# Kernel tuning notes

Hardware: AMD Instinct MI355X
Metric: run time of the kernel (lower is better)

Reference implementation:

```python
import jax, jax.numpy as jnp
import numpy as np

COMMITMENT_COST = 0.25
NUM_EMBEDDINGS = 512
EMBEDDING_DIM = 128


def setup_inputs() -> dict:
    key = jax.random.key(0)
    k1, k2 = jax.random.split(key)
    z = jax.random.normal(k1, (64, 128, 32, 32), dtype=jnp.float32)
    # nn.Embedding weight initialized uniform(-1/K, 1/K)
    lim = 1.0 / NUM_EMBEDDINGS
    emb_weight = jax.random.uniform(
        k2, (NUM_EMBEDDINGS, EMBEDDING_DIM), dtype=jnp.float32,
        minval=-lim, maxval=lim)
    return {"z": z, "emb_weight": emb_weight}


def reference(z, emb_weight):
    b, c, h, w = z.shape  # c == embedding_dim
    # (b, h, w, c) -> (b*h*w, c)
    z_cl = jnp.transpose(z, (0, 2, 3, 1))
    z_flat = z_cl.reshape(b * h * w, c)
    # squared L2 distances: ||z||^2 + ||e||^2 - 2 z.e  -> [N, K]
    distances = (
        jnp.sum(z_flat ** 2, axis=-1, keepdims=True)
        + jnp.sum(emb_weight ** 2, axis=-1)[None, :]
        - 2.0 * jnp.matmul(z_flat, emb_weight.T)
    )
    encoding_indices = jnp.argmin(distances, axis=-1)  # [N]
    z_q = emb_weight[encoding_indices]                 # [N, c]
    z_q = z_q.reshape(b, h, w, c)
    z_q = jnp.transpose(z_q, (0, 3, 1, 2))             # [b, c, h, w]
    loss = (
        jnp.mean((z_q - jax.lax.stop_gradient(z)) ** 2)
        + COMMITMENT_COST * jnp.mean((jax.lax.stop_gradient(z_q) - z) ** 2)
    )
    # straight-through estimator
    z_q_st = z + jax.lax.stop_gradient(z_q - z)
    return (z_q_st, loss, encoding_indices)
```

## Files before the change

### kernel.cpp

```cpp
#include <hip/hip_runtime.h>


#define D_DIM 128
#define HW    1024
#define GAP_THR 2.5e-4f
#define FLAG_CAP 16384

typedef short short8 __attribute__((ext_vector_type(8)));
typedef float f32x16 __attribute__((ext_vector_type(16)));

union U8 { unsigned int u[4]; short8 s; uint4 q; };

__device__ __forceinline__ unsigned short f2bf(float v) {
    unsigned int u = __builtin_bit_cast(unsigned int, v);
    return (unsigned short)((u + 0x7fffu + ((u >> 16) & 1u)) >> 16);
}
__device__ __forceinline__ float bfhi(unsigned short h) {
    unsigned int u = ((unsigned int)h) << 16;
    return __builtin_bit_cast(float, u);
}
__device__ __forceinline__ unsigned int umn(unsigned int a, unsigned int b) {
    return a < b ? a : b;
}
__device__ __forceinline__ unsigned int umx(unsigned int a, unsigned int b) {
    return a > b ? a : b;
}

__global__ void prep_kernel(const float* __restrict__ emb,
                            float* __restrict__ etr,
                            uint4* __restrict__ ebh, uint4* __restrict__ ebl,
                            float* __restrict__ se) {
    const int t = blockIdx.x * 256 + threadIdx.x;

    {
        const int k = t >> 7;
        const int d = t & 127;
        etr[d * 512 + k] = emb[t];
    }

    if (t < 8192) {
        const int lane = t & 63;
        const int ks   = (t >> 6) & 7;
        const int kcol = t >> 9;
        const int krow = kcol * 32 + (lane & 31);
        const int d0   = ks * 16 + (lane >> 5) * 8;
        const float* ep = emb + (size_t)krow * D_DIM + d0;
        float v[8];
        #pragma unroll
        for (int j = 0; j < 8; ++j) v[j] = ep[j];
        U8 hh, ll;
        #pragma unroll
        for (int p = 0; p < 4; ++p) {
            const unsigned short h0 = f2bf(v[2*p]), h1 = f2bf(v[2*p+1]);
            const unsigned short l0 = f2bf(v[2*p]   - bfhi(h0));
            const unsigned short l1 = f2bf(v[2*p+1] - bfhi(h1));
            hh.u[p] = (unsigned int)h0 | ((unsigned int)h1 << 16);
            ll.u[p] = (unsigned int)l0 | ((unsigned int)l1 << 16);
        }
        ebh[t] = hh.q;
        ebl[t] = ll.q;
    }

    if (t < 512) {
        const float* e = emb + (size_t)t * D_DIM;
        float r[8];
        #pragma unroll
        for (int j = 0; j < 8; ++j) {
            float v = e[j];
            float p = v * v;
            asm("" : "+v"(p));
            r[j] = p;
        }
        for (int i = 8; i < 128; i += 8) {
            #pragma unroll
            for (int j = 0; j < 8; ++j) {
                float v = e[i + j];
                float p = v * v;
                asm("" : "+v"(p));
                r[j] += p;
            }
        }
        se[t] = ((r[0] + r[1]) + (r[2] + r[3])) + ((r[4] + r[5]) + (r[6] + r[7]));
    }
}

__launch_bounds__(256, 1)
__global__ void dist_kernel(const float* __restrict__ z,
                            const uint4* __restrict__ ebh,
                            const uint4* __restrict__ ebl,
                            const float* __restrict__ se_g,
                            const float* __restrict__ emb,
                            float* __restrict__ idx_out,
                            unsigned int* __restrict__ flag_cnt,
                            int* __restrict__ flag_list,
                            float* __restrict__ zq,
                            double* __restrict__ loss) {
    __shared__ unsigned int red1[2][64], red2[2][64];
    __shared__ int   li_sh[64];
    __shared__ float ept[D_DIM * 33];
    __shared__ float lred[4];

    const int tid  = threadIdx.x;
    const int lane = tid & 63;
    const int wid  = tid >> 6;
    const int wn   = wid >> 1;
    const int wk   = wid & 1;
    const int row  = lane & 31;
    const int bidl = (int)blockIdx.x;
    const int bid  = (bidl & 7) * 128 + (bidl >> 3);
    const int nblk = bid * 64;
    const int bimg = nblk >> 10;
    const int hw0  = nblk & 1023;
    const int hww  = hw0 + wn * 32;

    short8 Ah[8], Al[8];
    {
        const float* zc = z + (size_t)bimg * (D_DIM * HW) + hww + row;
        #pragma unroll
        for (int ks = 0; ks < 8; ++ks) {
            const int d0 = ks * 16 + (lane >> 5) * 8;
            float v[8];
            #pragma unroll
            for (int j = 0; j < 8; ++j) v[j] = zc[(size_t)(d0 + j) * HW];
            U8 hh, ll;
            #pragma unroll
            for (int p = 0; p < 4; ++p) {
                unsigned int hwd, lwd;
                asm("v_cvt_pk_bf16_f32 %0, %1, %2" : "=v"(hwd) : "v"(v[2*p]), "v"(v[2*p+1]));
                const float xh = __builtin_bit_cast(float, hwd << 16);
                const float yh = __builtin_bit_cast(float, hwd & 0xffff0000u);
                const float xl = v[2*p]   - xh;
                const float yl = v[2*p+1] - yh;
                asm("v_cvt_pk_bf16_f32 %0, %1, %2" : "=v"(lwd) : "v"(xl), "v"(yl));
                hh.u[p] = hwd; ll.u[p] = lwd;
            }
            Ah[ks] = hh.s; Al[ks] = ll.s;
        }
    }

    unsigned int b1[16], b2[16];
    #pragma unroll
    for (int j = 0; j < 16; ++j) { b1[j] = 0xFFFFFFFFu; b2[j] = 0xFFFFFFFFu; }

    for (int i = 0; i < 8; ++i) {
        const int   kc   = wk * 8 + i;
        const int   kgl  = kc * 32 + row;
        const float sevp = se_g[kgl] + 0.5f;
        const uint4* pbh = ebh + kc * 512 + lane;
        const uint4* pbl = ebl + kc * 512 + lane;

        f32x16 ahh, ahl, alh;
        #pragma unroll
        for (int j = 0; j < 16; ++j) { ahh[j] = 0.f; ahl[j] = 0.f; alh[j] = 0.f; }

        __builtin_amdgcn_s_setprio(1);
        #pragma unroll
        for (int ks = 0; ks < 8; ++ks) {
            U8 bh; bh.q = pbh[ks * 64];
            U8 bl; bl.q = pbl[ks * 64];
            ahh = __builtin_amdgcn_mfma_f32_32x32x16_bf16(Ah[ks], bh.s, ahh, 0, 0, 0);
            ahl = __builtin_amdgcn_mfma_f32_32x32x16_bf16(Ah[ks], bl.s, ahl, 0, 0, 0);
            alh = __builtin_amdgcn_mfma_f32_32x32x16_bf16(Al[ks], bh.s, alh, 0, 0, 0);
        }
        __builtin_amdgcn_s_setprio(0);

        #pragma unroll
        for (int j = 0; j < 16; ++j) {
            const float pd = fmaf(-2.f, ahh[j],
                             fmaf(-2.f, ahl[j],
                             fmaf(-2.f, alh[j], sevp)));
            const unsigned int key =
                (__builtin_bit_cast(unsigned int, pd) & 0xFFFFFE00u) | (unsigned int)kgl;
            const unsigned int m = umn(key, b1[j]);
            b2[j] = umn(umx(key, b1[j]), b2[j]);
            b1[j] = m;
        }
    }

    #pragma unroll
    for (int off = 1; off <= 16; off <<= 1) {
        #pragma unroll
        for (int j = 0; j < 16; ++j) {
            const unsigned int o1 = (unsigned int)__shfl_xor((int)b1[j], off);
            const unsigned int o2 = (unsigned int)__shfl_xor((int)b2[j], off);
            const unsigned int m  = umn(b1[j], o1);
            b2[j] = umn(umx(b1[j], o1), umn(b2[j], o2));
            b1[j] = m;
        }
    }

    if ((lane & 31) == 0) {
        const int half = lane >> 5;
        #pragma unroll
        for (int j = 0; j < 16; ++j) {
            const int r = wn * 32 + (j & 3) + 8 * (j >> 2) + 4 * half;
            red1[wk][r] = b1[j];
            red2[wk][r] = b2[j];
        }
    }
    __syncthreads();

    if (tid < 64) {
        const unsigned int v1a = red1[0][tid], v2a = red2[0][tid];
        const unsigned int v1b = red1[1][tid], v2b = red2[1][tid];
        const unsigned int m1 = umn(v1a, v1b);
        const unsigned int m2 = umn(umn(v2a, v2b), umx(v1a, v1b));
        const int n = nblk + tid;
        const int code = (int)(m1 & 511u);
        idx_out[n] = (float)code;
        li_sh[tid] = code;
        const float f1 = __builtin_bit_cast(float, m1 & 0xFFFFFE00u);
        const float f2 = __builtin_bit_cast(float, m2 & 0xFFFFFE00u);
        if (f2 - f1 < GAP_THR) {
            unsigned int p = atomicAdd(flag_cnt, 1u);
            if (p < FLAG_CAP) flag_list[p] = n;
        }
    }

    float lacc = 0.f;
    for (int h = 0; h < 2; ++h) {
        __syncthreads();
        {
            const int p   = tid >> 3;
            const int sub = tid & 7;
            const float* er = emb + (size_t)li_sh[h * 32 + p] * D_DIM + sub * 16;
            #pragma unroll
            for (int j4 = 0; j4 < 4; ++j4) {
                const float4 v = *(const float4*)(er + j4 * 4);
                const int c = sub * 16 + j4 * 4;
                ept[(c + 0) * 33 + p] = v.x;
                ept[(c + 1) * 33 + p] = v.y;
                ept[(c + 2) * 33 + p] = v.z;
                ept[(c + 3) * 33 + p] = v.w;
            }
        }
        __syncthreads();
        {
            const int p  = tid & 31;
            const int c0 = tid >> 5;
            const int hwp = hw0 + h * 32 + p;
            const float* zb2 = z  + (size_t)bimg * (D_DIM * HW) + hwp;
            float*       qb  = zq + (size_t)bimg * (D_DIM * HW) + hwp;
            #pragma unroll
            for (int i = 0; i < 16; ++i) {
                const int c = c0 + i * 8;
                const float v  = ept[c * 33 + p];
                const float zv = zb2[(size_t)c * HW];
                qb[(size_t)c * HW] = v;
                const float df = v - zv;
                lacc = fmaf(df, df, lacc);
            }
        }
    }
    #pragma unroll
    for (int off = 32; off > 0; off >>= 1) lacc += __shfl_down(lacc, off);
    if (lane == 0) lred[wid] = lacc;
    __syncthreads();
    if (tid == 0)
        atomicAdd(loss, (double)(lred[0] + lred[1] + lred[2] + lred[3]));
}

__launch_bounds__(512)
__global__ void fixup_kernel(const float* __restrict__ z,
                             const float* __restrict__ etr,
                             const unsigned int* __restrict__ flag_cnt,
                             const int* __restrict__ flag_list,
                             const float* __restrict__ se_np,
                             float* __restrict__ idx_out) {
    __shared__ float zrow[D_DIM];
    __shared__ float q[D_DIM];
    __shared__ float rsum[8];
    __shared__ float szs;
    __shared__ float rv[8];
    __shared__ int   rix[8];

    const int tid = threadIdx.x;
    unsigned int cnt = *flag_cnt;
    if (cnt > FLAG_CAP) cnt = FLAG_CAP;

    for (unsigned int f = blockIdx.x; f < cnt; f += gridDim.x) {
        const int row = flag_list[f];
        const int b   = row >> 10;
        const int hw  = row & 1023;
        __syncthreads();
        if (tid < D_DIM) {
            float v = z[(size_t)b * (D_DIM * HW) + (size_t)tid * HW + hw];
            zrow[tid] = v;
            q[tid] = v * v;
        }
        __syncthreads();
        if (tid < 8) {
            float r = q[tid];
            for (int i = 8; i < 128; i += 8) r += q[i + tid];
            rsum[tid] = r;
        }
        __syncthreads();
        if (tid == 0)
            szs = ((rsum[0] + rsum[1]) + (rsum[2] + rsum[3]))
                + ((rsum[4] + rsum[5]) + (rsum[6] + rsum[7]));
        __syncthreads();
        const float sz32 = szs;

        const int k = tid;
        double dot0 = 0.0, dot1 = 0.0;
        #pragma unroll 4
        for (int d = 0; d < D_DIM; d += 2) {
            dot0 += (double)etr[d * 512 + k]       * (double)zrow[d];
            dot1 += (double)etr[(d + 1) * 512 + k] * (double)zrow[d + 1];
        }
        const float dotf = (float)(dot0 + dot1);
        const float T    = sz32 + se_np[k];
        float best  = T - 2.0f * dotf;
        int   besti = k;

        #pragma unroll
        for (int off = 32; off > 0; off >>= 1) {
            const float ov = __shfl_down(best, off);
            const int   oi = __shfl_down(besti, off);
            if (ov < best || (ov == best && oi < besti)) { best = ov; besti = oi; }
        }
        if ((tid & 63) == 0) { rv[tid >> 6] = best; rix[tid >> 6] = besti; }
        __syncthreads();
        if (tid == 0) {
            #pragma unroll
            for (int w = 1; w < 8; ++w)
                if (rv[w] < best || (rv[w] == best && rix[w] < besti)) {
                    best = rv[w]; besti = rix[w];
                }
            idx_out[row] = (float)besti;
        }
    }
}

__global__ void fin_kernel(const double* __restrict__ loss, float* __restrict__ out_loss) {
    *out_loss = (float)(*loss * 1.25 / 8388608.0);
}

extern "C" void kernel_launch(void* const* d_in, const int* in_sizes, int n_in,
                              void* d_out, int out_size, void* d_ws, size_t ws_size,
                              hipStream_t stream) {
    const float* z   = (const float*)d_in[0];
    const float* emb = (const float*)d_in[1];
    float* out      = (float*)d_out;
    float* zq       = out;
    float* out_loss = out + 8388608;
    float* idx_f    = out + 8388609;

    char* ws = (char*)d_ws;
    unsigned int* flag_cnt = (unsigned int*)ws;
    double*       loss     = (double*)(ws + 8);
    float*        se       = (float*)(ws + 10240);
    uint4*        ebh      = (uint4*)(ws + 16384);
    uint4*        ebl      = (uint4*)(ws + 16384 + 131072);
    int*          flag_list= (int*)(ws + 16384 + 262144);
    float*        etr      = (float*)(ws + 16384 + 262144 + 65536);

    hipMemsetAsync(d_ws, 0, 16384, stream);
    prep_kernel <<<256,  256, 0, stream>>>(emb, etr, ebh, ebl, se);
    dist_kernel <<<1024, 256, 0, stream>>>(z, ebh, ebl, se, emb, idx_f,
                                           flag_cnt, flag_list, zq, loss);
    fixup_kernel<<<2048, 512, 0, stream>>>(z, etr, flag_cnt, flag_list, se, idx_f);
    fin_kernel  <<<1,    1,   0, stream>>>(loss, out_loss);
}
```

Before: 100.3 us.

## Drop split-bf16 correction terms, use single bf16 MFMA with wider fixup gap

Replaces the three-term hi/lo bf16 split matmul with a single bf16 MFMA per k-step, removing the low-part embedding buffer and the low-part z conversion. The near-tie threshold for the exact fp32 fixup pass is widened to cover the larger bf16 error. Launch bounds are raised to allow higher occupancy, and the codebook chunk order is rotated per block to spread cache traffic. The risk is that more rows get flagged for fixup, possibly overflowing the flag capacity, which would hurt correctness or move cost into the fixup kernel.

Result: no change. 98.89 us, median of 2 (-1.4%).

```diff
diff --git a/kernel.cpp b/kernel.cpp
--- a/kernel.cpp
+++ b/kernel.cpp
@@ -3,7 +3,7 @@
 
 #define D_DIM 128
 #define HW    1024
-#define GAP_THR 2.5e-4f
+#define GAP_THR 4e-4f
 #define FLAG_CAP 16384
 
 typedef short short8 __attribute__((ext_vector_type(8)));
@@ -15,10 +15,6 @@
     unsigned int u = __builtin_bit_cast(unsigned int, v);
     return (unsigned short)((u + 0x7fffu + ((u >> 16) & 1u)) >> 16);
 }
-__device__ __forceinline__ float bfhi(unsigned short h) {
-    unsigned int u = ((unsigned int)h) << 16;
-    return __builtin_bit_cast(float, u);
-}
 __device__ __forceinline__ unsigned int umn(unsigned int a, unsigned int b) {
     return a < b ? a : b;
 }
@@ -28,7 +24,7 @@
 
 __global__ void prep_kernel(const float* __restrict__ emb,
                             float* __restrict__ etr,
-                            uint4* __restrict__ ebh, uint4* __restrict__ ebl,
+                            uint4* __restrict__ ebh,
                             float* __restrict__ se) {
     const int t = blockIdx.x * 256 + threadIdx.x;
 
@@ -48,17 +44,13 @@
         float v[8];
         #pragma unroll
         for (int j = 0; j < 8; ++j) v[j] = ep[j];
-        U8 hh, ll;
+        U8 hh;
         #pragma unroll
         for (int p = 0; p < 4; ++p) {
             const unsigned short h0 = f2bf(v[2*p]), h1 = f2bf(v[2*p+1]);
-            const unsigned short l0 = f2bf(v[2*p]   - bfhi(h0));
-            const unsigned short l1 = f2bf(v[2*p+1] - bfhi(h1));
             hh.u[p] = (unsigned int)h0 | ((unsigned int)h1 << 16);
-            ll.u[p] = (unsigned int)l0 | ((unsigned int)l1 << 16);
         }
         ebh[t] = hh.q;
-        ebl[t] = ll.q;
     }
 
     if (t < 512) {
@@ -84,10 +76,9 @@
     }
 }
 
-__launch_bounds__(256, 1)
+__launch_bounds__(256, 4)
 __global__ void dist_kernel(const float* __restrict__ z,
                             const uint4* __restrict__ ebh,
-                            const uint4* __restrict__ ebl,
                             const float* __restrict__ se_g,
                             const float* __restrict__ emb,
                             float* __restrict__ idx_out,
@@ -113,7 +104,7 @@
     const int hw0  = nblk & 1023;
     const int hww  = hw0 + wn * 32;
 
-    short8 Ah[8], Al[8];
+    short8 Ah[8];
     {
         const float* zc = z + (size_t)bimg * (D_DIM * HW) + hww + row;
         #pragma unroll
@@ -122,19 +113,14 @@
             float v[8];
             #pragma unroll
             for (int j = 0; j < 8; ++j) v[j] = zc[(size_t)(d0 + j) * HW];
-            U8 hh, ll;
+            U8 hh;
             #pragma unroll
             for (int p = 0; p < 4; ++p) {
-                unsigned int hwd, lwd;
+                unsigned int hwd;
                 asm("v_cvt_pk_bf16_f32 %0, %1, %2" : "=v"(hwd) : "v"(v[2*p]), "v"(v[2*p+1]));
-                const float xh = __builtin_bit_cast(float, hwd << 16);
-                const float yh = __builtin_bit_cast(float, hwd & 0xffff0000u);
-                const float xl = v[2*p]   - xh;
-                const float yl = v[2*p+1] - yh;
-                asm("v_cvt_pk_bf16_f32 %0, %1, %2" : "=v"(lwd) : "v"(xl), "v"(yl));
-                hh.u[p] = hwd; ll.u[p] = lwd;
+                hh.u[p] = hwd;
             }
-            Ah[ks] = hh.s; Al[ks] = ll.s;
+            Ah[ks] = hh.s;
         }
     }
 
@@ -143,32 +129,26 @@
     for (int j = 0; j < 16; ++j) { b1[j] = 0xFFFFFFFFu; b2[j] = 0xFFFFFFFFu; }
 
     for (int i = 0; i < 8; ++i) {
-        const int   kc   = wk * 8 + i;
+        const int   kc   = wk * 8 + ((i + bidl) & 7);
         const int   kgl  = kc * 32 + row;
         const float sevp = se_g[kgl] + 0.5f;
         const uint4* pbh = ebh + kc * 512 + lane;
-        const uint4* pbl = ebl + kc * 512 + lane;
-
-        f32x16 ahh, ahl, alh;
-        #pragma unroll
-        for (int j = 0; j < 16; ++j) { ahh[j] = 0.f; ahl[j] = 0.f; alh[j] = 0.f; }
+
+        f32x16 acc;
+        #pragma unroll
+        for (int j = 0; j < 16; ++j) acc[j] = 0.f;
 
         __builtin_amdgcn_s_setprio(1);
         #pragma unroll
         for (int ks = 0; ks < 8; ++ks) {
             U8 bh; bh.q = pbh[ks * 64];
-            U8 bl; bl.q = pbl[ks * 64];
-            ahh = __builtin_amdgcn_mfma_f32_32x32x16_bf16(Ah[ks], bh.s, ahh, 0, 0, 0);
-            ahl = __builtin_amdgcn_mfma_f32_32x32x16_bf16(Ah[ks], bl.s, ahl, 0, 0, 0);
-            alh = __builtin_amdgcn_mfma_f32_32x32x16_bf16(Al[ks], bh.s, alh, 0, 0, 0);
+            acc = __builtin_amdgcn_mfma_f32_32x32x16_bf16(Ah[ks], bh.s, acc, 0, 0, 0);
         }
         __builtin_amdgcn_s_setprio(0);
 
         #pragma unroll
         for (int j = 0; j < 16; ++j) {
-            const float pd = fmaf(-2.f, ahh[j],
-                             fmaf(-2.f, ahl[j],
-                             fmaf(-2.f, alh[j], sevp)));
+            const float pd = fmaf(-2.f, acc[j], sevp);
             const unsigned int key =
                 (__builtin_bit_cast(unsigned int, pd) & 0xFFFFFE00u) | (unsigned int)kgl;
             const unsigned int m = umn(key, b1[j]);
@@ -351,13 +331,12 @@
     double*       loss     = (double*)(ws + 8);
     float*        se       = (float*)(ws + 10240);
     uint4*        ebh      = (uint4*)(ws + 16384);
-    uint4*        ebl      = (uint4*)(ws + 16384 + 131072);
     int*          flag_list= (int*)(ws + 16384 + 262144);
     float*        etr      = (float*)(ws + 16384 + 262144 + 65536);
 
     hipMemsetAsync(d_ws, 0, 16384, stream);
-    prep_kernel <<<256,  256, 0, stream>>>(emb, etr, ebh, ebl, se);
-    dist_kernel <<<1024, 256, 0, stream>>>(z, ebh, ebl, se, emb, idx_f,
+    prep_kernel <<<256,  256, 0, stream>>>(emb, etr, ebh, se);
+    dist_kernel <<<1024, 256, 0, stream>>>(z, ebh, se, emb, idx_f,
                                            flag_cnt, flag_list, zq, loss);
     fixup_kernel<<<2048, 512, 0, stream>>>(z, etr, flag_cnt, flag_list, se, idx_f);
     fin_kernel  <<<1,    1,   0, stream>>>(loss, out_loss);
```
